# Kernel optimization log

Hardware: AMD Instinct MI355X
Metric: run time of the kernel (lower is better)

The kernel has to match this reference:

```python
import jax, jax.numpy as jnp
import numpy as np

B, S, Dm = 2, 4096, 1024
H, HD = 8, 128            # num_heads, head_dim
WIN, STRIDE = 512, 256    # window_size, window_size // 2
NGT = 64                  # num_global_tokens


def setup_inputs() -> dict:
    key = jax.random.key(0)
    ks = jax.random.split(key, 6)
    sc = lambda k, shape: jax.random.normal(k, shape, jnp.float32) * 0.02
    return {
        "hidden_states": jax.random.normal(ks[0], (B, S, Dm), jnp.float32),
        "global_memory": jax.random.normal(ks[1], (1, H, NGT, HD), jnp.float32),
        "conv_w": sc(ks[2], (Dm, Dm, 4)),   # (out_ch, in_ch, kernel)
        "conv_b": jnp.zeros((Dm,), jnp.float32),
        "mix_w": sc(ks[3], (2 * Dm, Dm)),
        "mix_b": jnp.zeros((Dm,), jnp.float32),
        "out_w": sc(ks[4], (Dm, Dm)),
        "out_b": jnp.zeros((Dm,), jnp.float32),
    }


def _sliding_window(x):
    nw = (S - WIN) // STRIDE + 1
    idx = np.arange(nw)[:, None] * STRIDE + np.arange(WIN)[None, :]
    w = x[:, idx, :].reshape(B, nw, WIN, H, HD)
    att = jnp.einsum('bnqhd,bnkhd->bnhqk', w, w) / np.sqrt(HD).astype(np.float32)
    att = jax.nn.softmax(att, axis=-1)
    o = jnp.einsum('bnhqk,bnkhd->bnqhd', att, w).reshape(B, nw, WIN, Dm)
    # triangular-weighted overlap-add (every window has full length here)
    tri = jnp.linspace(0.5, 1.5, WIN, dtype=x.dtype)
    contrib = (o * tri[None, None, :, None]).reshape(B, nw * WIN, Dm)
    ids = jnp.asarray(idx.reshape(-1))
    num = jax.ops.segment_sum(jnp.moveaxis(contrib, 1, 0), ids, num_segments=S)  # (S,B,Dm)
    den = jax.ops.segment_sum(jnp.tile(tri, nw), ids, num_segments=S)            # (S,)
    return jnp.moveaxis(num, 0, 1) / jnp.maximum(den, 1e-6)[None, :, None]


def _compressed_global(x, gmem, cw, cb):
    # Conv1d(k=4, stride=4) == blockwise contraction over non-overlapping groups of 4
    comp = jnp.einsum('btkd,odk->bto', x.reshape(B, S // 4, 4, Dm), cw) + cb
    comp = comp[:, :NGT].reshape(B, NGT, H, HD).transpose(0, 2, 1, 3)  # (B,H,NGT,HD)
    kv = jnp.concatenate([comp, jnp.broadcast_to(gmem, (B, H, NGT, HD))], axis=2)
    q = x.reshape(B, S, H, HD).transpose(0, 2, 1, 3)                    # (B,H,S,HD)
    att = jax.nn.softmax(jnp.einsum('bhsd,bhtd->bhst', q, kv) / np.sqrt(HD).astype(np.float32), axis=-1)
    out = jnp.einsum('bhst,bhtd->bhsd', att, kv)
    return out.transpose(0, 2, 1, 3).reshape(B, S, Dm)


def _broadcast(x):
    # exponential diffusion: O(log n) roll steps (12 for S=4096)
    result = jnp.zeros_like(x)
    cur = x
    stride = 1
    while stride < S:
        cur = cur + 0.5 * (jnp.roll(cur, stride, axis=1) + jnp.roll(cur, -stride, axis=1))
        result = result + cur
        stride *= 2
    return result / np.float32(np.log2(S) + 1.0)


def reference(hidden_states, global_memory, conv_w, conv_b, mix_w, mix_b, out_w, out_b):
    local = _sliding_window(hidden_states)
    glob = _compressed_global(hidden_states, global_memory, conv_w, conv_b)
    bc = _broadcast(hidden_states)
    gate = jax.nn.sigmoid(jnp.concatenate([local, glob], axis=-1) @ mix_w + mix_b)
    mixed = gate * local + (1.0 - gate) * glob + bc
    return mixed @ out_w + out_b
```

## Files before the change

kernel.cpp:

```cpp
#include <hip/hip_runtime.h>
#include <cstdint>

#define B_   2
#define S_   4096
#define DM   1024
#define NH   8
#define HDIM 128
#define NWIN 15

typedef __attribute__((ext_vector_type(8))) short s8v;
typedef __attribute__((ext_vector_type(4))) float f4v;

__device__ __forceinline__ float f_lo(unsigned int u){
  union { unsigned int i; float f; } v; v.i = u << 16; return v.f;
}
__device__ __forceinline__ float f_hi(unsigned int u){
  union { unsigned int i; float f; } v; v.i = u & 0xffff0000u; return v.f;
}
__device__ __forceinline__ unsigned short f2bf(float f){
  unsigned int x = __float_as_uint(f);
  x += 0x7fffu + ((x >> 16) & 1u);
  return (unsigned short)(x >> 16);
}
__device__ __forceinline__ unsigned int pack2(float a, float b){
  return (unsigned int)f2bf(a) | ((unsigned int)f2bf(b) << 16);
}

__global__ __launch_bounds__(256) void k_cvtbf(const float* __restrict__ src,
                                               unsigned short* __restrict__ dst){
  size_t i = ((size_t)blockIdx.x*256 + threadIdx.x)*8;
  float4 a = *(const float4*)(src + i);
  float4 b = *(const float4*)(src + i + 4);
  uint4 r; r.x = pack2(a.x,a.y); r.y = pack2(a.z,a.w);
  r.z = pack2(b.x,b.y); r.w = pack2(b.z,b.w);
  *(uint4*)(dst + i) = r;
}

__global__ __launch_bounds__(256) void k_xposef(const float* __restrict__ x,
                                                float* __restrict__ xT){
  __shared__ float Ls[64][68];
  const int bid = blockIdx.x;
  const int b = bid>>10, r = bid&1023, st = r>>4, dt = r&15;
  const int s0 = st*64, d0 = dt*64;
  const int tid = threadIdx.x;
#pragma unroll
  for(int p=0;p<4;p++){
    int rr = p*16 + (tid>>4), c4 = (tid&15)*4;
    *(float4*)&Ls[rr][c4] = *(const float4*)(x + ((size_t)(b*S_)+s0+rr)*DM + d0 + c4);
  }
  __syncthreads();
#pragma unroll
  for(int p=0;p<4;p++){
    int dr = p*16 + (tid>>4), c4 = (tid&15)*4;
    float4 v = { Ls[c4+0][dr], Ls[c4+1][dr], Ls[c4+2][dr], Ls[c4+3][dr] };
    *(float4*)(xT + ((size_t)(b*DM)+d0+dr)*S_ + s0 + c4) = v;
  }
}

__global__ __launch_bounds__(256) void k_diffuseT(const float* __restrict__ xT,
                                                  unsigned short* __restrict__ bcT){
  __shared__ float bufA[2][4096];
  __shared__ float bufB[2][4096];
  const int b  = blockIdx.x >> 9;
  const int d0 = (blockIdx.x & 511) * 2;
  const int tid = threadIdx.x;
  float cur[32], res[32];
#pragma unroll
  for(int k=0;k<32;k++){
    int e = tid + (k<<8); int ch = e>>12; int s = e&4095;
    float v = xT[((size_t)(b*DM)+d0+ch)*S_ + s];
    cur[k] = v; res[k] = 0.f; bufA[ch][s] = v;
  }
  __syncthreads();
#pragma unroll 1
  for(int st=0; st<12; st++){
    const int stride = 1<<st;
    float (*src)[4096] = (st&1) ? bufB : bufA;
    float (*dst)[4096] = (st&1) ? bufA : bufB;
#pragma unroll
    for(int k=0;k<32;k++){
      int e = tid + (k<<8); int ch=e>>12; int s=e&4095;
      float c = cur[k] + 0.5f*(src[ch][(s-stride)&4095] + src[ch][(s+stride)&4095]);
      dst[ch][s] = c; cur[k] = c; res[k] += c;
    }
    __syncthreads();
  }
#pragma unroll
  for(int k=0;k<32;k++){
    int e = tid + (k<<8); int ch=e>>12; int s=e&4095;
    bcT[((size_t)(b*DM)+d0+ch)*S_ + s] = f2bf(res[k]*(1.0f/13.0f));
  }
}

__global__ __launch_bounds__(256) void k_bcxpose(const unsigned short* __restrict__ bcT,
                                                 unsigned short* __restrict__ bc){
  __shared__ unsigned short Ls[64*72];
  const int bid = blockIdx.x;
  const int b = bid>>10, r = bid&1023, st = r>>4, dt = r&15;
  const int s0 = st*64, d0 = dt*64;
  const int tid = threadIdx.x;
#pragma unroll
  for(int t=0;t<2;t++){
    int cl = tid + t*256; int dr = cl>>3, c = cl&7;
    *(uint4*)&Ls[dr*72 + c*8] = *(const uint4*)(bcT + ((size_t)(b*DM)+d0+dr)*S_ + s0 + c*8);
  }
  __syncthreads();
#pragma unroll
  for(int t=0;t<2;t++){
    int cl = tid + t*256; int sr = cl>>3, c = cl&7;
    unsigned short tmp[8];
#pragma unroll
    for(int j=0;j<8;j++) tmp[j] = Ls[(c*8+j)*72 + sr];
    *(uint4*)(bc + ((size_t)(b*S_)+s0+sr)*DM + d0 + c*8) = *(const uint4*)tmp;
  }
}

__global__ __launch_bounds__(256) void k_xstage(const float* __restrict__ x,
                                                unsigned short* __restrict__ Asta){
  __shared__ float xs[4][1024];
  const int m = blockIdx.x;
  const int b = m>>6, t = m&63;
  const int tid = threadIdx.x;
  const float* xp = x + (size_t)(b*S_ + 4*t)*DM;
  for(int i=tid; i<4096; i+=256) xs[i>>10][i&1023] = xp[i];
  __syncthreads();
  float v[16];
#pragma unroll
  for(int e=0; e<16; e++) v[e] = xs[e&3][tid*4 + (e>>2)];
  uint4 r0, r1;
  r0.x = pack2(v[0],v[1]);  r0.y = pack2(v[2],v[3]);
  r0.z = pack2(v[4],v[5]);  r0.w = pack2(v[6],v[7]);
  r1.x = pack2(v[8],v[9]);  r1.y = pack2(v[10],v[11]);
  r1.z = pack2(v[12],v[13]); r1.w = pack2(v[14],v[15]);
  unsigned short* op = Asta + (size_t)m*4096 + tid*16;
  *(uint4*)op = r0;
  *(uint4*)(op+8) = r1;
}

__global__ __launch_bounds__(256) void k_gemmconv(const unsigned short* __restrict__ A,
                                                  const unsigned short* __restrict__ Bw,
                                                  float* __restrict__ part){
  __shared__ __align__(16) unsigned short As[128*64];
  __shared__ __align__(16) unsigned short Bs[128*64];
  const int nt = blockIdx.x, kt = blockIdx.y;
  const int n0 = nt<<7;
  const int tid = threadIdx.x, wid = tid>>6, lane = tid&63, quad = lane>>4, tl = lane&15;
  const int mq = (wid&1)*64, nq = (wid>>1)*64;
  f4v acc[4][4];
#pragma unroll
  for(int i=0;i<4;i++)
#pragma unroll
    for(int j=0;j<4;j++) acc[i][j] = (f4v)(0.f);

  for(int kc=kt*1024; kc<kt*1024+1024; kc+=64){
    __syncthreads();
#pragma unroll
    for(int t=0; t<4; t++){
      int cl = tid + t*256, m = cl>>3, c = cl&7;
      uint4 v = *(const uint4*)(A + (size_t)m*4096 + kc + c*8);
      *(uint4*)&As[m*64 + ((c ^ (m&7))<<3)] = v;
      uint4 w = *(const uint4*)(Bw + (size_t)(n0+m)*4096 + kc + c*8);
      *(uint4*)&Bs[m*64 + ((c ^ (m&7))<<3)] = w;
    }
    __syncthreads();
#pragma unroll
    for(int ks=0; ks<2; ks++){
      s8v af[4], bf[4];
#pragma unroll
      for(int i=0;i<4;i++){
        int ml = mq + i*16 + tl;
        af[i] = *(const s8v*)&As[ml*64 + (((ks*4+quad) ^ (ml&7))<<3)];
      }
#pragma unroll
      for(int j=0;j<4;j++){
        int nl = nq + j*16 + tl;
        bf[j] = *(const s8v*)&Bs[nl*64 + (((ks*4+quad) ^ (nl&7))<<3)];
      }
#pragma unroll
      for(int i=0;i<4;i++)
#pragma unroll
        for(int j=0;j<4;j++)
          acc[i][j] = __builtin_amdgcn_mfma_f32_16x16x32_bf16(af[i], bf[j], acc[i][j], 0, 0, 0);
    }
  }
  float* pp = part + (size_t)kt*131072;
#pragma unroll
  for(int i=0;i<4;i++)
#pragma unroll
    for(int r=0;r<4;r++){
      int m = mq + i*16 + quad*4 + r;
#pragma unroll
      for(int j=0;j<4;j++){
        int n = n0 + nq + j*16 + tl;
        pp[m*1024 + n] = acc[i][j][r];
      }
    }
}

__global__ __launch_bounds__(256) void k_convred(const float* __restrict__ part,
                                                 const float* __restrict__ cb,
                                                 unsigned short* __restrict__ kv){
  int i = blockIdx.x*256 + threadIdx.x;
  int m = i>>10, o = i&1023;
  float v = part[i] + part[131072+i] + part[262144+i] + part[393216+i] + cb[o];
  int b = m>>6, t = m&63, h = o>>7, hd = o&127;
  kv[((size_t)(b*NH + h)*128 + t)*HDIM + hd] = f2bf(v);
}

__global__ __launch_bounds__(256) void k_gmem(const float* __restrict__ g,
                                              unsigned short* __restrict__ kv){
  int i = blockIdx.x*256 + threadIdx.x;
  int hd = i & 127, gt = (i>>7)&63, h = (i>>13)&7, b = i>>16;
  kv[((size_t)(b*NH + h)*128 + 64 + gt)*HDIM + hd] = f2bf(g[((size_t)(h*64 + gt))*HDIM + hd]);
}

template<int MODE>
__global__ __launch_bounds__(256, 3) void k_attn(const unsigned short* __restrict__ xb,
                                                 const unsigned short* __restrict__ kvb,
                                                 unsigned short* __restrict__ outb){
  __shared__ __align__(16) unsigned short sh[25600];
  constexpr int KSo = 0;
  constexpr int VTo = 8192;
  constexpr int PSo = 17408;

  const int b = blockIdx.y;
  int h, n, qt, nkt;
  if(MODE==0){ int r = blockIdx.x; n = r>>5; h = (r>>2)&7; qt = r&3; nkt = 8; }
  else       { int r = blockIdx.x; h = r>>5; qt = r&31; n = 0; nkt = 2; }

  const int tid  = threadIdx.x;
  const int wid  = tid>>6, lane = tid&63, quad = lane>>4, tl = lane&15;
  const int sQ   = (MODE==0) ? (n*256 + qt*128) : (qt*128);

  s8v qf[2][4];
#pragma unroll
  for(int qi=0; qi<2; qi++){
    int qr = sQ + wid*32 + qi*16 + tl;
    const unsigned short* qp = xb + ((size_t)(b*S_) + qr)*DM + h*HDIM;
#pragma unroll
    for(int ks=0; ks<4; ks++)
      qf[qi][ks] = *(const s8v*)(qp + ks*32 + quad*8);
  }

  const unsigned short* kbase = (MODE==0)
      ? xb + ((size_t)(b*S_) + n*256)*DM + h*HDIM
      : kvb + (size_t)(b*NH+h)*128*HDIM;
  const int kstride = (MODE==0) ? DM : HDIM;
  const int mrow = (tid&15)*4;
  const int cg   = tid>>4;

  uint4 rg[4];
#pragma unroll
  for(int j=0;j<4;j++)
    rg[j] = *(const uint4*)(kbase + (size_t)(mrow+j)*kstride + cg*8);

  f4v oacc[8][2];
#pragma unroll
  for(int ht=0; ht<8; ht++){ oacc[ht][0] = (f4v)(0.f); oacc[ht][1] = (f4v)(0.f); }
  float m_[2] = {-1e30f, -1e30f}, l_[2] = {0.f, 0.f};

  const float SC2 = 0.12751743f;

  for(int kt=0; kt<nkt; kt++){
    __syncthreads();
#pragma unroll
    for(int j=0;j<4;j++){
      int t = mrow + j;
      *(uint4*)&sh[KSo + t*128 + ((cg ^ (t&7))<<3)] = rg[j];
    }
    {
      const unsigned int* w0 = (const unsigned int*)&rg[0];
      const unsigned int* w1 = (const unsigned int*)&rg[1];
      const unsigned int* w2 = (const unsigned int*)&rg[2];
      const unsigned int* w3 = (const unsigned int*)&rg[3];
#pragma unroll
      for(int i=0;i<8;i++){
        int w = i>>1;
        unsigned int a, c2;
        if(i&1){ a  = (w0[w]>>16) | (w1[w] & 0xffff0000u);
                 c2 = (w2[w]>>16) | (w3[w] & 0xffff0000u); }
        else   { a  = (w0[w] & 0xffffu) | (w1[w]<<16);
                 c2 = (w2[w] & 0xffffu) | (w3[w]<<16); }
        uint2 u = {a, c2};
        *(uint2*)&sh[VTo + (cg*8+i)*72 + mrow] = u;
      }
    }
    __syncthreads();
    if(kt+1 < nkt){
      const unsigned short* np = kbase + (size_t)((kt+1)*64 + mrow)*kstride + cg*8;
#pragma unroll
      for(int j=0;j<4;j++) rg[j] = *(const uint4*)(np + (size_t)j*kstride);
    }

    f4v st[4][2];
#pragma unroll
    for(int tt=0; tt<4; tt++){
      st[tt][0] = (f4v)(0.f); st[tt][1] = (f4v)(0.f);
      int row = tt*16 + tl;
#pragma unroll
      for(int ks=0; ks<4; ks++){
        s8v af = *(const s8v*)&sh[KSo + row*128 + (((ks*4+quad) ^ (row&7))<<3)];
        st[tt][0] = __builtin_amdgcn_mfma_f32_16x16x32_bf16(af, qf[0][ks], st[tt][0], 0, 0, 0);
        st[tt][1] = __builtin_amdgcn_mfma_f32_16x16x32_bf16(af, qf[1][ks], st[tt][1], 0, 0, 0);
      }
    }

#pragma unroll
    for(int qi=0; qi<2; qi++){
      float ma = fmaxf(fmaxf(st[0][qi][0],st[0][qi][1]), fmaxf(st[0][qi][2],st[0][qi][3]));
      float mb = fmaxf(fmaxf(st[1][qi][0],st[1][qi][1]), fmaxf(st[1][qi][2],st[1][qi][3]));
      float mc = fmaxf(fmaxf(st[2][qi][0],st[2][qi][1]), fmaxf(st[2][qi][2],st[2][qi][3]));
      float md = fmaxf(fmaxf(st[3][qi][0],st[3][qi][1]), fmaxf(st[3][qi][2],st[3][qi][3]));
      float mx = fmaxf(fmaxf(ma,mb), fmaxf(mc,md));
      mx = fmaxf(mx, __shfl_xor(mx, 16));
      mx = fmaxf(mx, __shfl_xor(mx, 32));
      if(!__all(mx <= m_[qi] + 60.0f)){
        float al = exp2f((m_[qi] - mx)*SC2);
        l_[qi] *= al;
#pragma unroll
        for(int ht=0; ht<8; ht++) oacc[ht][qi] *= al;
        m_[qi] = mx;
      }
      float mm = m_[qi];
      float ps = 0.f;
#pragma unroll
      for(int tt=0; tt<4; tt++)
#pragma unroll
        for(int r=0; r<4; r++){
          float p = exp2f((st[tt][qi][r] - mm)*SC2);
          st[tt][qi][r] = p; ps += p;
        }
      ps += __shfl_xor(ps, 16);
      ps += __shfl_xor(ps, 32);
      l_[qi] += ps;
      int ql = wid*32 + qi*16 + tl;
#pragma unroll
      for(int tt=0; tt<4; tt++){
        ushort4 u = { f2bf(st[tt][qi][0]), f2bf(st[tt][qi][1]),
                      f2bf(st[tt][qi][2]), f2bf(st[tt][qi][3]) };
        *(ushort4*)&sh[PSo + ql*64 + (((tt*2 + (quad>>1)) ^ (ql&7))<<3) + (quad&1)*4] = u;
      }
    }

#pragma unroll
    for(int kk=0; kk<2; kk++){
      int ql0 = wid*32 + tl, ql1 = wid*32 + 16 + tl;
      s8v pb0 = *(const s8v*)&sh[PSo + ql0*64 + (((kk*4+quad) ^ (ql0&7))<<3)];
      s8v pb1 = *(const s8v*)&sh[PSo + ql1*64 + (((kk*4+quad) ^ (ql1&7))<<3)];
#pragma unroll
      for(int ht=0; ht<8; ht++){
        s8v vf = *(const s8v*)&sh[VTo + (ht*16 + tl)*72 + kk*32 + quad*8];
        oacc[ht][0] = __builtin_amdgcn_mfma_f32_16x16x32_bf16(vf, pb0, oacc[ht][0], 0, 0, 0);
        oacc[ht][1] = __builtin_amdgcn_mfma_f32_16x16x32_bf16(vf, pb1, oacc[ht][1], 0, 0, 0);
      }
    }
  }

#pragma unroll
  for(int qi=0; qi<2; qi++){
    float inv = 1.0f/l_[qi];
#pragma unroll
    for(int ht=0; ht<8; ht++) oacc[ht][qi] *= inv;
  }
  __syncthreads();
#pragma unroll
  for(int qi=0; qi<2; qi++){
    int ql = wid*32 + qi*16 + tl;
#pragma unroll
    for(int ht=0; ht<8; ht++){
      ushort4 u = { f2bf(oacc[ht][qi][0]), f2bf(oacc[ht][qi][1]),
                    f2bf(oacc[ht][qi][2]), f2bf(oacc[ht][qi][3]) };
      *(ushort4*)&sh[ql*136 + ht*16 + quad*4] = u;
    }
  }
  __syncthreads();
  {
    int ql = tid>>1, half = tid&1;
    size_t row = (MODE==0) ? (size_t)((b*NWIN + n)*512 + qt*128 + ql)
                           : (size_t)(b*S_ + qt*128 + ql);
    unsigned short* op = outb + row*DM + h*HDIM + half*64;
#pragma unroll
    for(int c=0; c<8; c++){
      uint4 v = *(const uint4*)&sh[ql*136 + half*64 + c*8];
      *(uint4*)(op + c*8) = v;
    }
  }
}

__global__ __launch_bounds__(256) void k_combine(const unsigned short* __restrict__ wso,
                                                 unsigned short* __restrict__ loc){
  const int bid = blockIdx.x;
  const int b = bid >> 12, s = bid & 4095;
  const int tid = threadIdx.x;
  const int nhi = s >> 8, sl = s & 255;
  const int c0 = tid*4;
  float n0=0.f, n1=0.f, n2=0.f, n3=0.f, den=0.f;
  if(nhi <= 14){
    float tr = 0.5f + (float)sl*(1.0f/511.0f);
    den += tr;
    uint2 u = *(const uint2*)(wso + (size_t)((b*NWIN + nhi)*512 + sl)*DM + c0);
    n0 += tr*f_lo(u.x); n1 += tr*f_hi(u.x); n2 += tr*f_lo(u.y); n3 += tr*f_hi(u.y);
  }
  if(nhi >= 1){
    int q2 = sl + 256;
    float tr = 0.5f + (float)q2*(1.0f/511.0f);
    den += tr;
    uint2 u = *(const uint2*)(wso + (size_t)((b*NWIN + nhi-1)*512 + q2)*DM + c0);
    n0 += tr*f_lo(u.x); n1 += tr*f_hi(u.x); n2 += tr*f_lo(u.y); n3 += tr*f_hi(u.y);
  }
  float di = 1.0f/den;
  uint2 o; o.x = pack2(n0*di, n1*di); o.y = pack2(n2*di, n3*di);
  *(uint2*)(loc + (size_t)(b*S_ + s)*DM + c0) = o;
}

__global__ __launch_bounds__(256) void k_wcvt(const float* __restrict__ W,
                                              unsigned short* __restrict__ WT, int K){
  __shared__ float Ls[64][68];
  int kt = blockIdx.x >> 4, nt = blockIdx.x & 15;
  int k0 = kt<<6, n0 = nt<<6;
  int tid = threadIdx.x;
#pragma unroll
  for(int p=0; p<4; p++){
    int r = p*16 + (tid>>4), c4 = (tid&15)*4;
    float4 v = *(const float4*)(W + (size_t)(k0+r)*1024 + n0 + c4);
    *(float4*)&Ls[r][c4] = v;
  }
  __syncthreads();
  int nn = tid>>2, kq = tid&3;
#pragma unroll
  for(int c=0; c<4; c++){
    int k = kq*16 + c*4;
    ushort4 u = { f2bf(Ls[k+0][nn]), f2bf(Ls[k+1][nn]), f2bf(Ls[k+2][nn]), f2bf(Ls[k+3][nn]) };
    *(ushort4*)(WT + (size_t)(n0+nn)*K + k0 + k) = u;
  }
}

template<int MODE>
__global__ __launch_bounds__(256) void k_gemm2(const unsigned short* __restrict__ A0,
                                               const unsigned short* __restrict__ A1,
                                               const unsigned short* __restrict__ WT,
                                               const float* __restrict__ bias,
                                               const unsigned short* __restrict__ loc,
                                               const unsigned short* __restrict__ glo,
                                               const unsigned short* __restrict__ bcb,
                                               unsigned short* __restrict__ outb,
                                               float* __restrict__ outf){
  const int KTOT = (MODE==0) ? 2048 : 1024;
  __shared__ __align__(16) unsigned short As[128*64];
  __shared__ __align__(16) unsigned short Bs[128*64];
  const int mt = blockIdx.x >> 3, nt = blockIdx.x & 7;
  const int m0 = mt<<7, n0 = nt<<7;
  const int tid = threadIdx.x, wid = tid>>6, lane = tid&63, quad = lane>>4, tl = lane&15;
  const int mq = (wid&1)*64, nq = (wid>>1)*64;
  f4v acc[4][4];
#pragma unroll
  for(int i=0;i<4;i++)
#pragma unroll
    for(int j=0;j<4;j++) acc[i][j] = (f4v)(0.f);

  for(int kc=0; kc<KTOT; kc+=64){
    __syncthreads();
    const unsigned short* Ab = (MODE==0 && kc>=1024) ? A1 : A0;
    const int kb = (MODE==0) ? (kc & 1023) : kc;
#pragma unroll
    for(int t=0; t<4; t++){
      int cl = tid + t*256, m = cl>>3, c = cl&7;
      uint4 v = *(const uint4*)(Ab + (size_t)(m0+m)*1024 + kb + c*8);
      *(uint4*)&As[m*64 + ((c ^ (m&7))<<3)] = v;
      uint4 w = *(const uint4*)(WT + (size_t)(n0+m)*KTOT + kc + c*8);
      *(uint4*)&Bs[m*64 + ((c ^ (m&7))<<3)] = w;
    }
    __syncthreads();
#pragma unroll
    for(int ks=0; ks<2; ks++){
      s8v af[4], bf[4];
#pragma unroll
      for(int i=0;i<4;i++){
        int ml = mq + i*16 + tl;
        af[i] = *(const s8v*)&As[ml*64 + (((ks*4+quad) ^ (ml&7))<<3)];
      }
#pragma unroll
      for(int j=0;j<4;j++){
        int nl = nq + j*16 + tl;
        bf[j] = *(const s8v*)&Bs[nl*64 + (((ks*4+quad) ^ (nl&7))<<3)];
      }
#pragma unroll
      for(int i=0;i<4;i++)
#pragma unroll
        for(int j=0;j<4;j++)
          acc[i][j] = __builtin_amdgcn_mfma_f32_16x16x32_bf16(af[i], bf[j], acc[i][j], 0, 0, 0);
    }
  }

#pragma unroll
  for(int i=0;i<4;i++){
#pragma unroll
    for(int r=0;r<4;r++){
      int m = m0 + mq + i*16 + quad*4 + r;
      size_t rowb = (size_t)m * 1024;
#pragma unroll
      for(int j=0;j<4;j++){
        int nn = n0 + nq + j*16 + tl;
        float v = acc[i][j][r] + bias[nn];
        if(MODE==0){
          float g  = 1.0f/(1.0f + __expf(-v));
          float lv = f_lo((unsigned int)loc[rowb+nn]);
          float gv = f_lo((unsigned int)glo[rowb+nn]);
          float bv = f_lo((unsigned int)bcb[rowb+nn]);
          outb[rowb+nn] = f2bf(g*lv + (1.0f-g)*gv + bv);
        } else {
          outf[rowb+nn] = v;
        }
      }
    }
  }
}

extern "C" void kernel_launch(void* const* d_in, const int* in_sizes, int n_in,
                              void* d_out, int out_size, void* d_ws, size_t ws_size,
                              hipStream_t stream){
  const float* x  = (const float*)d_in[0];
  const float* gm = (const float*)d_in[1];
  const float* cw = (const float*)d_in[2];
  const float* cb = (const float*)d_in[3];
  const float* mw = (const float*)d_in[4];
  const float* mb = (const float*)d_in[5];
  const float* ow = (const float*)d_in[6];
  const float* ob = (const float*)d_in[7];
  float* out = (float*)d_out;

  char* ws = (char*)d_ws;
  const size_t SZ = (size_t)B_*S_*DM*2;
  unsigned short* localb = (unsigned short*)(ws);
  unsigned short* globb  = (unsigned short*)(ws + SZ);
  unsigned short* bcb    = (unsigned short*)(ws + 2*SZ);
  unsigned short* kvb    = (unsigned short*)(ws + 3*SZ);
  unsigned short* wso    = (unsigned short*)(ws + 3*SZ + 524288);
  unsigned short* mixed  = wso;
  unsigned short* wt1    = (unsigned short*)(ws + 3*SZ + 524288 + SZ);
  unsigned short* wt2    = (unsigned short*)(ws + 3*SZ + 524288 + SZ + 4194304);
  unsigned short* cwb    = (unsigned short*)(ws);
  unsigned short* asta   = (unsigned short*)(ws + 8388608);
  float*          cpart  = (float*)        (ws + 9437184);
  float*          xT     = (float*)(ws + SZ);
  unsigned short* bcT    = wso;
  unsigned short* xbf    = (unsigned short*)(ws);

  k_cvtbf   <<<2048, 256, 0, stream>>>(cw, cwb);
  k_xstage  <<<128,  256, 0, stream>>>(x, asta);
  k_gemmconv<<<dim3(8,4), 256, 0, stream>>>(asta, cwb, cpart);
  k_convred <<<512,  256, 0, stream>>>(cpart, cb, kvb);
  k_gmem    <<<512,  256, 0, stream>>>(gm, kvb);
  k_xposef  <<<2048, 256, 0, stream>>>(x, xT);
  k_diffuseT<<<1024, 256, 0, stream>>>(xT, bcT);
  k_bcxpose <<<2048, 256, 0, stream>>>(bcT, bcb);
  k_cvtbf   <<<4096, 256, 0, stream>>>(x, xbf);
  k_attn<1> <<<dim3(256,2), 256, 0, stream>>>(xbf, kvb, globb);
  k_attn<0> <<<dim3(480,2), 256, 0, stream>>>(xbf, kvb, wso);
  k_combine <<<8192, 256, 0, stream>>>(wso, localb);
  k_wcvt    <<<512,  256, 0, stream>>>(mw, wt1, 2048);
  k_wcvt    <<<256,  256, 0, stream>>>(ow, wt2, 1024);
  k_gemm2<0><<<512, 256, 0, stream>>>(localb, globb, wt1, mb, localb, globb, bcb, mixed, nullptr);
  k_gemm2<1><<<512, 256, 0, stream>>>(mixed, nullptr, wt2, ob, nullptr, nullptr, nullptr, nullptr, out);
}
```

Before: 416.2 us.

## Double attention query tile per block to share K/V staging across 8 waves

Each attention block now uses 512 threads and covers 256 query rows instead of 128, so every staged K tile and transposed V tile in shared memory serves twice as many queries. This halves the number of blocks and the global-to-LDS K/V traffic per query. Block indices are also remapped with a modulo-8 swizzle, apparently to spread neighbouring windows and heads across XCDs. In exchange, shared memory per block grows and the tighter launch bound (4 waves per EU) may cap registers and cause spills or lower occupancy.

```diff
diff --git a/kernel.cpp b/kernel.cpp
--- a/kernel.cpp
+++ b/kernel.cpp
@@ -215,22 +215,29 @@
 }
 
 template<int MODE>
-__global__ __launch_bounds__(256, 3) void k_attn(const unsigned short* __restrict__ xb,
+__global__ __launch_bounds__(512, 4) void k_attn(const unsigned short* __restrict__ xb,
                                                  const unsigned short* __restrict__ kvb,
                                                  unsigned short* __restrict__ outb){
-  __shared__ __align__(16) unsigned short sh[25600];
+  __shared__ __align__(16) unsigned short sh[34816];
   constexpr int KSo = 0;
   constexpr int VTo = 8192;
   constexpr int PSo = 17408;
 
   const int b = blockIdx.y;
-  int h, n, qt, nkt;
-  if(MODE==0){ int r = blockIdx.x; n = r>>5; h = (r>>2)&7; qt = r&3; nkt = 8; }
-  else       { int r = blockIdx.x; h = r>>5; qt = r&31; n = 0; nkt = 2; }
+  int h, n, h2, nkt;
+  if(MODE==0){
+    int r = blockIdx.x;
+    int s = (r&7)*30 + (r>>3);
+    n = s>>4; h = (s>>1)&7; h2 = s&1; nkt = 8;
+  } else {
+    int r = blockIdx.x;
+    int s = (r&7)*16 + (r>>3);
+    h = s>>4; h2 = s&15; n = 0; nkt = 2;
+  }
 
   const int tid  = threadIdx.x;
   const int wid  = tid>>6, lane = tid&63, quad = lane>>4, tl = lane&15;
-  const int sQ   = (MODE==0) ? (n*256 + qt*128) : (qt*128);
+  const int sQ   = (MODE==0) ? (n*256 + h2*256) : (h2*256);
 
   s8v qf[2][4];
 #pragma unroll
@@ -246,13 +253,12 @@
       ? xb + ((size_t)(b*S_) + n*256)*DM + h*HDIM
       : kvb + (size_t)(b*NH+h)*128*HDIM;
   const int kstride = (MODE==0) ? DM : HDIM;
-  const int mrow = (tid&15)*4;
-  const int cg   = tid>>4;
-
-  uint4 rg[4];
-#pragma unroll
-  for(int j=0;j<4;j++)
-    rg[j] = *(const uint4*)(kbase + (size_t)(mrow+j)*kstride + cg*8);
+  const int mrow = (tid&31)*2;
+  const int cg   = tid>>5;
+
+  uint4 rg[2];
+  rg[0] = *(const uint4*)(kbase + (size_t)mrow*kstride + cg*8);
+  rg[1] = *(const uint4*)(kbase + (size_t)(mrow+1)*kstride + cg*8);
 
   f4v oacc[8][2];
 #pragma unroll
@@ -264,32 +270,26 @@
   for(int kt=0; kt<nkt; kt++){
     __syncthreads();
 #pragma unroll
-    for(int j=0;j<4;j++){
+    for(int j=0;j<2;j++){
       int t = mrow + j;
       *(uint4*)&sh[KSo + t*128 + ((cg ^ (t&7))<<3)] = rg[j];
     }
     {
       const unsigned int* w0 = (const unsigned int*)&rg[0];
       const unsigned int* w1 = (const unsigned int*)&rg[1];
-      const unsigned int* w2 = (const unsigned int*)&rg[2];
-      const unsigned int* w3 = (const unsigned int*)&rg[3];
 #pragma unroll
       for(int i=0;i<8;i++){
         int w = i>>1;
-        unsigned int a, c2;
-        if(i&1){ a  = (w0[w]>>16) | (w1[w] & 0xffff0000u);
-                 c2 = (w2[w]>>16) | (w3[w] & 0xffff0000u); }
-        else   { a  = (w0[w] & 0xffffu) | (w1[w]<<16);
-                 c2 = (w2[w] & 0xffffu) | (w3[w]<<16); }
-        uint2 u = {a, c2};
-        *(uint2*)&sh[VTo + (cg*8+i)*72 + mrow] = u;
+        unsigned int a = (i&1) ? ((w0[w]>>16) | (w1[w] & 0xffff0000u))
+                               : ((w0[w] & 0xffffu) | (w1[w]<<16));
+        *(unsigned int*)&sh[VTo + (cg*8+i)*72 + mrow] = a;
       }
     }
     __syncthreads();
     if(kt+1 < nkt){
       const unsigned short* np = kbase + (size_t)((kt+1)*64 + mrow)*kstride + cg*8;
-#pragma unroll
-      for(int j=0;j<4;j++) rg[j] = *(const uint4*)(np + (size_t)j*kstride);
+      rg[0] = *(const uint4*)np;
+      rg[1] = *(const uint4*)(np + kstride);
     }
 
     f4v st[4][2];
@@ -376,8 +376,8 @@
   __syncthreads();
   {
     int ql = tid>>1, half = tid&1;
-    size_t row = (MODE==0) ? (size_t)((b*NWIN + n)*512 + qt*128 + ql)
-                           : (size_t)(b*S_ + qt*128 + ql);
+    size_t row = (MODE==0) ? ((size_t)(b*NWIN + n)*512 + h2*256 + ql)
+                           : ((size_t)(b*S_) + h2*256 + ql);
     unsigned short* op = outb + row*DM + h*HDIM + half*64;
 #pragma unroll
     for(int c=0; c<8; c++){
@@ -555,8 +555,8 @@
   k_diffuseT<<<1024, 256, 0, stream>>>(xT, bcT);
   k_bcxpose <<<2048, 256, 0, stream>>>(bcT, bcb);
   k_cvtbf   <<<4096, 256, 0, stream>>>(x, xbf);
-  k_attn<1> <<<dim3(256,2), 256, 0, stream>>>(xbf, kvb, globb);
-  k_attn<0> <<<dim3(480,2), 256, 0, stream>>>(xbf, kvb, wso);
+  k_attn<1> <<<dim3(128,2), 512, 0, stream>>>(xbf, kvb, globb);
+  k_attn<0> <<<dim3(240,2), 512, 0, stream>>>(xbf, kvb, wso);
   k_combine <<<8192, 256, 0, stream>>>(wso, localb);
   k_wcvt    <<<512,  256, 0, stream>>>(mw, wt1, 2048);
   k_wcvt    <<<256,  256, 0, stream>>>(ow, wt2, 1024);
```

Result: slower. 462.8 us (+11.2%).
